# Performance work log

Measured on AMD Instinct MI355X. Metric: run time of the kernel, lower is better.

The kernel has to match this reference:

```python
import jax, jax.numpy as jnp
import numpy as np

MAX_REL = 2  # hard-coded max_relative_position in the torch module


def setup_inputs() -> dict:
    key = jax.random.key(0)
    ks = jax.random.split(key, 12)
    B, S, Dm, H = 2, 2048, 1024, 16
    D = Dm // H
    sc = 1.0 / np.sqrt(Dm)
    inp = {
        "x": jax.random.normal(ks[0], (B, S, Dm), jnp.float32),
        "Wq": jax.random.normal(ks[1], (Dm, Dm), jnp.float32) * sc,
        "bq": jnp.zeros((Dm,), jnp.float32),
        "Wk": jax.random.normal(ks[2], (Dm, Dm), jnp.float32) * sc,
        "bk": jnp.zeros((Dm,), jnp.float32),
        "Wv": jax.random.normal(ks[3], (Dm, Dm), jnp.float32) * sc,
        "bv": jnp.zeros((Dm,), jnp.float32),
        "Wo": jax.random.normal(ks[4], (Dm, Dm), jnp.float32) * sc,
        "bo": jnp.zeros((Dm,), jnp.float32),
        "rel_k": jax.random.normal(ks[5], (2 * MAX_REL + 1, D), jnp.float32) * 0.1,
        "rel_v": jax.random.normal(ks[6], (2 * MAX_REL + 1, D), jnp.float32) * 0.1,
        "num_heads": H,
    }
    return inp


def reference(x, Wq, bq, Wk, bk, Wv, bv, Wo, bo, rel_k, rel_v, num_heads):
    B, S, Dm = x.shape
    H = num_heads
    D = Dm // H
    n_buckets = 2 * MAX_REL + 1

    q = (x @ Wq + bq).reshape(B, S, H, D).transpose(0, 2, 1, 3)  # [B,H,S,D]
    k = (x @ Wk + bk).reshape(B, S, H, D).transpose(0, 2, 1, 3)
    v = (x @ Wv + bv).reshape(B, S, H, D).transpose(0, 2, 1, 3)

    # content-content scores
    attn1 = jnp.einsum('bhqd,bhkd->bhqk', q, k)

    # relative-position bucket index: clip(k - q, -MAX_REL, MAX_REL) + MAX_REL
    r = jnp.arange(S)
    idx = jnp.clip(r[None, :] - r[:, None], -MAX_REL, MAX_REL) + MAX_REL  # [S,S] int

    # content-position scores: q . rel_k[idx]  (project onto 5 buckets then gather)
    q_rel = jnp.einsum('bhqd,jd->bhqj', q, rel_k)  # [B,H,S,5]
    attn2 = jnp.take_along_axis(q_rel, jnp.broadcast_to(idx[None, None], (B, H, S, S)), axis=-1)

    scores = (attn1 + attn2) / jnp.sqrt(jnp.asarray(D, x.dtype))
    p = jax.nn.softmax(scores, axis=-1)  # dropout in eval mode -> identity

    out1 = jnp.einsum('bhqk,bhkd->bhqd', p, v)

    # position value term: sum_k p[...,k] * rel_v[idx[q,k]] via bucket accumulation
    onehot = (idx[:, :, None] == jnp.arange(n_buckets)[None, None, :]).astype(p.dtype)  # [S,S,5]
    bucket = jnp.einsum('bhqk,qkj->bhqj', p, onehot)
    out2 = jnp.einsum('bhqj,jd->bhqd', bucket, rel_v)

    out = (out1 + out2).transpose(0, 2, 1, 3).reshape(B, S, Dm)
    return out @ Wo + bo
```

## Files before the change

### kernel.cpp

```cpp
#include <hip/hip_runtime.h>

#define S_LEN 2048
#define DM    1024
#define NH    16
#define HD    64
#define BATCH 2
#define PPAD  2056

typedef __attribute__((ext_vector_type(8))) short short8;
typedef __attribute__((ext_vector_type(4))) float f32x4;

__device__ inline float b2f(unsigned short u) {
    return __uint_as_float(((unsigned)u) << 16);
}
__device__ inline unsigned short f2b(float f) {
    unsigned u = __float_as_uint(f);
    u += 0x7FFFu + ((u >> 16) & 1u);
    return (unsigned short)(u >> 16);
}
__device__ inline f32x4 zero4() {
    f32x4 z; z[0] = 0.f; z[1] = 0.f; z[2] = 0.f; z[3] = 0.f; return z;
}

__device__ inline size_t qk_frag_idx(int s, int d) {
    return (size_t)(s >> 4) * 1024 + (size_t)(d >> 5) * 512
         + (size_t)(((d & 31) >> 3) * 16 + (s & 15)) * 8 + (d & 7);
}
__device__ inline size_t v_frag_idx(int s, int d) {
    return (size_t)(s >> 5) * 2048 + (size_t)(d >> 4) * 512
         + (size_t)(((s & 31) >> 3) * 16 + (d & 15)) * 8 + (s & 7);
}
__device__ inline size_t af_idx(int m, int k) {
    return ((size_t)(m >> 4) * 32 + (size_t)(k >> 5)) * 512
         + (size_t)(((k & 31) >> 3) * 16 + (m & 15)) * 8 + (k & 7);
}

__global__ __launch_bounds__(256) void convert_w(
    const float* __restrict__ Wq, const float* __restrict__ Wk,
    const float* __restrict__ Wv, const float* __restrict__ Wo,
    unsigned short* __restrict__ Wf)
{
    int k = blockIdx.x, mat = blockIdx.y, tid = threadIdx.x;
    const float* W = (mat == 0) ? Wq : (mat == 1) ? Wk : (mat == 2) ? Wv : Wo;
    f32x4 w = *(const f32x4*)(W + (size_t)k * DM + tid * 4);
    unsigned short* dst = Wf + ((size_t)mat << 20);
#pragma unroll
    for (int e = 0; e < 4; e++) dst[af_idx(tid * 4 + e, k)] = f2b(w[e]);
}

__global__ __launch_bounds__(256) void convert_x(
    const float* __restrict__ x, unsigned short* __restrict__ Xf, int b)
{
    int m = blockIdx.x, tid = threadIdx.x;
    f32x4 v = *(const f32x4*)(x + ((size_t)b * S_LEN + m) * DM + tid * 4);
#pragma unroll
    for (int e = 0; e < 4; e++) Xf[af_idx(m, tid * 4 + e)] = f2b(v[e]);
}

__global__ __launch_bounds__(256) void proj_gemm_wf(
    const unsigned short* __restrict__ Xf,
    const unsigned short* __restrict__ Wf,
    const float* __restrict__ bq, const float* __restrict__ bk,
    const float* __restrict__ bv,
    unsigned short* __restrict__ Qs, unsigned short* __restrict__ Ks,
    unsigned short* __restrict__ Vts)
{
    int tid = threadIdx.x;
    int wave = tid >> 6, lane = tid & 63;
    int r = lane & 15, quad = lane >> 4;
    int mat = blockIdx.y >> 4;
    int hh  = blockIdx.y & 15;

    int mt0 = blockIdx.x * 8 + wave * 2;
    const unsigned short* A0 = Xf + (size_t)mt0 * 32 * 512 + lane * 8;
    const unsigned short* A1 = A0 + 32 * 512;
    const unsigned short* Bb = Wf + ((size_t)mat << 20)
                             + (size_t)(hh * 4) * 32 * 512 + lane * 8;

    f32x4 acc[2][4];
#pragma unroll
    for (int mt = 0; mt < 2; mt++)
#pragma unroll
        for (int nt = 0; nt < 4; nt++) acc[mt][nt] = zero4();

    short8 a0c = *(const short8*)A0;
    short8 a1c = *(const short8*)A1;
    short8 b0c = *(const short8*)(Bb);
    short8 b1c = *(const short8*)(Bb + 16384);
    short8 b2c = *(const short8*)(Bb + 32768);
    short8 b3c = *(const short8*)(Bb + 49152);

    for (int kt = 0; kt < 32; kt++) {
        short8 a0n, a1n, b0n, b1n, b2n, b3n;
        if (kt < 31) {
            size_t off = (size_t)(kt + 1) * 512;
            a0n = *(const short8*)(A0 + off);
            a1n = *(const short8*)(A1 + off);
            b0n = *(const short8*)(Bb + off);
            b1n = *(const short8*)(Bb + 16384 + off);
            b2n = *(const short8*)(Bb + 32768 + off);
            b3n = *(const short8*)(Bb + 49152 + off);
        }
        acc[0][0] = __builtin_amdgcn_mfma_f32_16x16x32_bf16(a0c, b0c, acc[0][0], 0, 0, 0);
        acc[0][1] = __builtin_amdgcn_mfma_f32_16x16x32_bf16(a0c, b1c, acc[0][1], 0, 0, 0);
        acc[0][2] = __builtin_amdgcn_mfma_f32_16x16x32_bf16(a0c, b2c, acc[0][2], 0, 0, 0);
        acc[0][3] = __builtin_amdgcn_mfma_f32_16x16x32_bf16(a0c, b3c, acc[0][3], 0, 0, 0);
        acc[1][0] = __builtin_amdgcn_mfma_f32_16x16x32_bf16(a1c, b0c, acc[1][0], 0, 0, 0);
        acc[1][1] = __builtin_amdgcn_mfma_f32_16x16x32_bf16(a1c, b1c, acc[1][1], 0, 0, 0);
        acc[1][2] = __builtin_amdgcn_mfma_f32_16x16x32_bf16(a1c, b2c, acc[1][2], 0, 0, 0);
        acc[1][3] = __builtin_amdgcn_mfma_f32_16x16x32_bf16(a1c, b3c, acc[1][3], 0, 0, 0);
        a0c = a0n; a1c = a1n;
        b0c = b0n; b1c = b1n; b2c = b2n; b3c = b3n;
    }

    const float* bias = (mat == 0) ? bq : (mat == 1) ? bk : bv;
    size_t hbase = (size_t)hh * S_LEN * HD;
    int gc0 = hh * 64;
#pragma unroll
    for (int mt = 0; mt < 2; mt++) {
#pragma unroll
        for (int nt = 0; nt < 4; nt++) {
            int d = nt * 16 + r;
            float bb = bias[gc0 + d];
#pragma unroll
            for (int i = 0; i < 4; i++) {
                int s = blockIdx.x * 128 + wave * 32 + mt * 16 + quad * 4 + i;
                float v = acc[mt][nt][i] + bb;
                if (mat == 2)      Vts[hbase + v_frag_idx(s, d)] = f2b(v);
                else if (mat == 0) Qs [hbase + qk_frag_idx(s, d)] = f2b(v);
                else               Ks [hbase + qk_frag_idx(s, d)] = f2b(v);
            }
        }
    }
}

__global__ __launch_bounds__(256) void outproj_wf(
    const unsigned short* __restrict__ AOf,
    const unsigned short* __restrict__ Wof,
    const float* __restrict__ bo,
    float* __restrict__ out, int b)
{
    int tid = threadIdx.x;
    int wave = tid >> 6, lane = tid & 63;
    int r = lane & 15, quad = lane >> 4;

    int mt0 = blockIdx.x * 8 + wave * 2;
    const unsigned short* A0 = AOf + (size_t)mt0 * 32 * 512 + lane * 8;
    const unsigned short* A1 = A0 + 32 * 512;
    const unsigned short* Bb = Wof + (size_t)(blockIdx.y * 4) * 32 * 512 + lane * 8;

    f32x4 acc[2][4];
#pragma unroll
    for (int mt = 0; mt < 2; mt++)
#pragma unroll
        for (int nt = 0; nt < 4; nt++) acc[mt][nt] = zero4();

    short8 a0c = *(const short8*)A0;
    short8 a1c = *(const short8*)A1;
    short8 b0c = *(const short8*)(Bb);
    short8 b1c = *(const short8*)(Bb + 16384);
    short8 b2c = *(const short8*)(Bb + 32768);
    short8 b3c = *(const short8*)(Bb + 49152);

    for (int kt = 0; kt < 32; kt++) {
        short8 a0n, a1n, b0n, b1n, b2n, b3n;
        if (kt < 31) {
            size_t off = (size_t)(kt + 1) * 512;
            a0n = *(const short8*)(A0 + off);
            a1n = *(const short8*)(A1 + off);
            b0n = *(const short8*)(Bb + off);
            b1n = *(const short8*)(Bb + 16384 + off);
            b2n = *(const short8*)(Bb + 32768 + off);
            b3n = *(const short8*)(Bb + 49152 + off);
        }
        acc[0][0] = __builtin_amdgcn_mfma_f32_16x16x32_bf16(a0c, b0c, acc[0][0], 0, 0, 0);
        acc[0][1] = __builtin_amdgcn_mfma_f32_16x16x32_bf16(a0c, b1c, acc[0][1], 0, 0, 0);
        acc[0][2] = __builtin_amdgcn_mfma_f32_16x16x32_bf16(a0c, b2c, acc[0][2], 0, 0, 0);
        acc[0][3] = __builtin_amdgcn_mfma_f32_16x16x32_bf16(a0c, b3c, acc[0][3], 0, 0, 0);
        acc[1][0] = __builtin_amdgcn_mfma_f32_16x16x32_bf16(a1c, b0c, acc[1][0], 0, 0, 0);
        acc[1][1] = __builtin_amdgcn_mfma_f32_16x16x32_bf16(a1c, b1c, acc[1][1], 0, 0, 0);
        acc[1][2] = __builtin_amdgcn_mfma_f32_16x16x32_bf16(a1c, b2c, acc[1][2], 0, 0, 0);
        acc[1][3] = __builtin_amdgcn_mfma_f32_16x16x32_bf16(a1c, b3c, acc[1][3], 0, 0, 0);
        a0c = a0n; a1c = a1n;
        b0c = b0n; b1c = b1n; b2c = b2n; b3c = b3n;
    }

#pragma unroll
    for (int mt = 0; mt < 2; mt++) {
#pragma unroll
        for (int nt = 0; nt < 4; nt++) {
            int n = blockIdx.y * 64 + nt * 16 + r;
            float bb = bo[n];
#pragma unroll
            for (int i = 0; i < 4; i++) {
                int m = blockIdx.x * 128 + wave * 32 + mt * 16 + quad * 4 + i;
                out[((size_t)b * S_LEN + m) * DM + n] = acc[mt][nt][i] + bb;
            }
        }
    }
}

__global__ __launch_bounds__(256) void proj_fused_xf(
    const unsigned short* __restrict__ Xf,
    const float* __restrict__ Wq, const float* __restrict__ Wk,
    const float* __restrict__ Wv,
    const float* __restrict__ bq, const float* __restrict__ bk,
    const float* __restrict__ bv,
    unsigned short* __restrict__ Qs, unsigned short* __restrict__ Ks,
    unsigned short* __restrict__ Vts)
{
    __shared__ unsigned short Bs[64][72];

    int tid = threadIdx.x;
    int wave = tid >> 6, lane = tid & 63;
    int r = lane & 15, quad = lane >> 4;
    int m0 = blockIdx.x * 64 + wave * 16;
    int mat = blockIdx.y / NH;
    int hh  = blockIdx.y % NH;
    int gc0 = hh * 64;

    const float* W    = (mat == 0) ? Wq : (mat == 1) ? Wk : Wv;
    const float* bias = (mat == 0) ? bq : (mat == 1) ? bk : bv;

    f32x4 acc[4];
#pragma unroll
    for (int nt = 0; nt < 4; nt++) acc[nt] = zero4();

    int kr = tid >> 2;
    int nc = (tid & 3) * 16;
    const unsigned short* Af = Xf + (size_t)(blockIdx.x * 4 + wave) * 32 * 512 + lane * 8;

    for (int k0 = 0; k0 < DM; k0 += 64) {
        const f32x4* wr = (const f32x4*)(W + (size_t)(k0 + kr) * DM + gc0 + nc);
        f32x4 w0 = wr[0], w1 = wr[1], w2 = wr[2], w3 = wr[3];
        __syncthreads();
        Bs[nc +  0][kr] = f2b(w0[0]); Bs[nc +  1][kr] = f2b(w0[1]);
        Bs[nc +  2][kr] = f2b(w0[2]); Bs[nc +  3][kr] = f2b(w0[3]);
        Bs[nc +  4][kr] = f2b(w1[0]); Bs[nc +  5][kr] = f2b(w1[1]);
        Bs[nc +  6][kr] = f2b(w1[2]); Bs[nc +  7][kr] = f2b(w1[3]);
        Bs[nc +  8][kr] = f2b(w2[0]); Bs[nc +  9][kr] = f2b(w2[1]);
        Bs[nc + 10][kr] = f2b(w2[2]); Bs[nc + 11][kr] = f2b(w2[3]);
        Bs[nc + 12][kr] = f2b(w3[0]); Bs[nc + 13][kr] = f2b(w3[1]);
        Bs[nc + 14][kr] = f2b(w3[2]); Bs[nc + 15][kr] = f2b(w3[3]);
        __syncthreads();

#pragma unroll
        for (int ks = 0; ks < 2; ks++) {
            int kt = (k0 >> 5) + ks;
            short8 a = *(const short8*)(Af + (size_t)kt * 512);
#pragma unroll
            for (int nt = 0; nt < 4; nt++) {
                short8 bf = *(const short8*)&Bs[nt * 16 + r][ks * 32 + quad * 8];
                acc[nt] = __builtin_amdgcn_mfma_f32_16x16x32_bf16(a, bf, acc[nt], 0, 0, 0);
            }
        }
    }

    size_t hbase = (size_t)hh * S_LEN * HD;
#pragma unroll
    for (int nt = 0; nt < 4; nt++) {
        int d = nt * 16 + r;
        float bb = bias[gc0 + d];
#pragma unroll
        for (int i = 0; i < 4; i++) {
            int s = m0 + quad * 4 + i;
            float v = acc[nt][i] + bb;
            if (mat == 2)      Vts[hbase + v_frag_idx(s, d)] = f2b(v);
            else if (mat == 0) Qs [hbase + qk_frag_idx(s, d)] = f2b(v);
            else               Ks [hbase + qk_frag_idx(s, d)] = f2b(v);
        }
    }
}

__global__ __launch_bounds__(256) void proj_fused_legacy(
    const float* __restrict__ x,
    const float* __restrict__ Wq, const float* __restrict__ Wk,
    const float* __restrict__ Wv,
    const float* __restrict__ bq, const float* __restrict__ bk,
    const float* __restrict__ bv,
    unsigned short* __restrict__ Qs, unsigned short* __restrict__ Ks,
    unsigned short* __restrict__ Vts,
    int b, int head0, int NG)
{
    __shared__ unsigned short Bs[64][72];

    int tid = threadIdx.x;
    int wave = tid >> 6, lane = tid & 63;
    int r = lane & 15, quad = lane >> 4;
    int m0 = blockIdx.x * 64 + wave * 16;
    int mat = blockIdx.y / NG;
    int hh  = blockIdx.y % NG;
    int gc0 = (head0 + hh) * 64;

    const float* W    = (mat == 0) ? Wq : (mat == 1) ? Wk : Wv;
    const float* bias = (mat == 0) ? bq : (mat == 1) ? bk : bv;
    const float* xb = x + (size_t)b * S_LEN * DM;

    f32x4 acc[4];
#pragma unroll
    for (int nt = 0; nt < 4; nt++) acc[nt] = zero4();

    int kr = tid >> 2;
    int nc = (tid & 3) * 16;
    const float* am = xb + (size_t)(m0 + r) * DM + quad * 8;

    for (int k0 = 0; k0 < DM; k0 += 64) {
        const f32x4* wr = (const f32x4*)(W + (size_t)(k0 + kr) * DM + gc0 + nc);
        f32x4 w0 = wr[0], w1 = wr[1], w2 = wr[2], w3 = wr[3];
        __syncthreads();
        Bs[nc +  0][kr] = f2b(w0[0]); Bs[nc +  1][kr] = f2b(w0[1]);
        Bs[nc +  2][kr] = f2b(w0[2]); Bs[nc +  3][kr] = f2b(w0[3]);
        Bs[nc +  4][kr] = f2b(w1[0]); Bs[nc +  5][kr] = f2b(w1[1]);
        Bs[nc +  6][kr] = f2b(w1[2]); Bs[nc +  7][kr] = f2b(w1[3]);
        Bs[nc +  8][kr] = f2b(w2[0]); Bs[nc +  9][kr] = f2b(w2[1]);
        Bs[nc + 10][kr] = f2b(w2[2]); Bs[nc + 11][kr] = f2b(w2[3]);
        Bs[nc + 12][kr] = f2b(w3[0]); Bs[nc + 13][kr] = f2b(w3[1]);
        Bs[nc + 14][kr] = f2b(w3[2]); Bs[nc + 15][kr] = f2b(w3[3]);
        __syncthreads();

#pragma unroll
        for (int ks = 0; ks < 2; ks++) {
            const f32x4* ap = (const f32x4*)(am + k0 + ks * 32);
            f32x4 a0 = ap[0], a1 = ap[1];
            short8 a;
            a[0] = (short)f2b(a0[0]); a[1] = (short)f2b(a0[1]);
            a[2] = (short)f2b(a0[2]); a[3] = (short)f2b(a0[3]);
            a[4] = (short)f2b(a1[0]); a[5] = (short)f2b(a1[1]);
            a[6] = (short)f2b(a1[2]); a[7] = (short)f2b(a1[3]);
#pragma unroll
            for (int nt = 0; nt < 4; nt++) {
                short8 bf = *(const short8*)&Bs[nt * 16 + r][ks * 32 + quad * 8];
                acc[nt] = __builtin_amdgcn_mfma_f32_16x16x32_bf16(a, bf, acc[nt], 0, 0, 0);
            }
        }
    }

    size_t hbase = (size_t)hh * S_LEN * HD;
#pragma unroll
    for (int nt = 0; nt < 4; nt++) {
        int d = nt * 16 + r;
        float bb = bias[gc0 + d];
#pragma unroll
        for (int i = 0; i < 4; i++) {
            int s = m0 + quad * 4 + i;
            float v = acc[nt][i] + bb;
            if (mat == 2)      Vts[hbase + v_frag_idx(s, d)] = f2b(v);
            else if (mat == 0) Qs [hbase + qk_frag_idx(s, d)] = f2b(v);
            else               Ks [hbase + qk_frag_idx(s, d)] = f2b(v);
        }
    }
}

__global__ __launch_bounds__(1024, 8) void attn_mfma(
    const unsigned short* __restrict__ Q,
    const unsigned short* __restrict__ Km,
    const unsigned short* __restrict__ Vt,
    const float* __restrict__ relk,
    const float* __restrict__ relv,
    unsigned short* __restrict__ Aout,
    int col_base,
    int NG, int ao_frag)
{
    __shared__ alignas(16) unsigned short pmat[16][PPAD];
    __shared__ float qrel_s[16][5];
    __shared__ float relv_s[5][HD];
    __shared__ float rowstat[16][8];
    __shared__ float wden[16][16];
    __shared__ float wsuf[16][16];

    int tid = threadIdx.x;
    int wave = tid >> 6, lane = tid & 63;
    int r = lane & 15, quad = lane >> 4;

    int bid = blockIdx.x;
    int hh, jq;
    if (NG == 16) {
        int xcd = bid & 7, j = bid >> 3;
        hh = xcd + ((j >> 7) << 3);
        jq = j & 127;
    } else {
        hh = bid >> 7;
        jq = bid & 127;
    }
    int q0 = jq << 4;

    size_t qk_base = (size_t)hh * S_LEN * HD;
    size_t v_base  = (size_t)hh * S_LEN * HD;

    const unsigned short* qf = Q + qk_base + (size_t)(q0 >> 4) * 1024 + lane * 8;
    short8 aq0 = *(const short8*)qf;
    short8 aq1 = *(const short8*)(qf + 512);

    {
        int t2 = tid - 64;
        if (t2 >= 0 && t2 < 5 * HD) relv_s[t2 >> 6][t2 & 63] = relv[t2];
    }

    if (wave == 0) {
#pragma unroll
        for (int j = 0; j < 5; j++) {
            const f32x4* rk0 = (const f32x4*)(relk + j * HD + quad * 8);
            const f32x4* rk1 = (const f32x4*)(relk + j * HD + 32 + quad * 8);
            f32x4 r0a = rk0[0], r0b = rk0[1], r1a = rk1[0], r1b = rk1[1];
            float s = 0.f;
#pragma unroll
            for (int e = 0; e < 4; e++) {
                s += b2f((unsigned short)aq0[e])     * r0a[e];
                s += b2f((unsigned short)aq0[e + 4]) * r0b[e];
                s += b2f((unsigned short)aq1[e])     * r1a[e];
                s += b2f((unsigned short)aq1[e + 4]) * r1b[e];
            }
            s += __shfl_xor(s, 16);
            s += __shfl_xor(s, 32);
            if (quad == 0) qrel_s[r][j] = s;
        }
    }

    __syncthreads();

    float dpart[4] = {0.f, 0.f, 0.f, 0.f};
    float spart[4] = {0.f, 0.f, 0.f, 0.f};
    int rowq = quad * 4;

    const unsigned short* kb = Km + qk_base + (size_t)(wave * 8) * 1024 + lane * 8;
    short8 bk0 = *(const short8*)kb;
    short8 bk1 = *(const short8*)(kb + 512);

    for (int t = 0; t < 8; t++) {
        short8 nb0, nb1;
        if (t < 7) {
            const unsigned short* kn = kb + (size_t)(t + 1) * 1024;
            nb0 = *(const short8*)(kn);
            nb1 = *(const short8*)(kn + 512);
        }
        f32x4 a1 = zero4();
        a1 = __builtin_amdgcn_mfma_f32_16x16x32_bf16(aq0, bk0, a1, 0, 0, 0);
        a1 = __builtin_amdgcn_mfma_f32_16x16x32_bf16(aq1, bk1, a1, 0, 0, 0);
        int col = wave * 128 + t * 16 + r;
#pragma unroll
        for (int i = 0; i < 4; i++) {
            int row = rowq + i;
            int qglob = q0 + row;
            int del = min(2, max(-2, col - qglob));
            float s = (a1[i] + qrel_s[row][del + 2]) * 0.125f;
            float e = __expf(s);
            pmat[row][col] = f2b(e);
            dpart[i] += e;
            if (col >= qglob + 2) spart[i] += e;
        }
        bk0 = nb0; bk1 = nb1;
    }
#pragma unroll
    for (int off = 1; off <= 8; off <<= 1) {
#pragma unroll
        for (int i = 0; i < 4; i++) {
            dpart[i] += __shfl_xor(dpart[i], off);
            spart[i] += __shfl_xor(spart[i], off);
        }
    }
    if (r == 0) {
#pragma unroll
        for (int i = 0; i < 4; i++) {
            wden[wave][rowq + i] = dpart[i];
            wsuf[wave][rowq + i] = spart[i];
        }
    }
    __syncthreads();

    if (tid < 16) {
        int row = tid, qglob = q0 + row;
        float denom = 0.f, suf = 0.f;
        for (int w = 0; w < 16; w++) { denom += wden[w][row]; suf += wsuf[w][row]; }
        float b1  = (qglob >= 1) ? b2f(pmat[row][qglob - 1]) : 0.f;
        float b2v = b2f(pmat[row][qglob]);
        float b3  = (qglob + 1 < S_LEN) ? b2f(pmat[row][qglob + 1]) : 0.f;
        rowstat[row][0] = 1.f / denom;
        rowstat[row][1] = denom - suf - b1 - b2v - b3;
        rowstat[row][2] = b1;
        rowstat[row][3] = b2v;
        rowstat[row][4] = b3;
        rowstat[row][5] = suf;
    }
    __syncthreads();

    {
        int nt = wave & 3, kc = wave >> 2;
        f32x4 oacc = zero4();
        const unsigned short* vf = Vt + v_base + (size_t)(kc * 16) * 2048
                                 + (size_t)nt * 512 + lane * 8;
        short8 af = *(const short8*)&pmat[r][kc * 512 + quad * 8];
        short8 bv = *(const short8*)vf;
        for (int st = 0; st < 16; st++) {
            short8 afn, bvn;
            if (st < 15) {
                afn = *(const short8*)&pmat[r][kc * 512 + (st + 1) * 32 + quad * 8];
                bvn = *(const short8*)(vf + (size_t)(st + 1) * 2048);
            }
            oacc = __builtin_amdgcn_mfma_f32_16x16x32_bf16(af, bv, oacc, 0, 0, 0);
            af = afn; bv = bvn;
        }
        __syncthreads();
        float* pbuf = (float*)&pmat[0][0];
#pragma unroll
        for (int i = 0; i < 4; i++)
            pbuf[((size_t)kc * 16 + quad * 4 + i) * 65 + nt * 16 + r] = oacc[i];
    }
    __syncthreads();

    {
        const float* pbuf = (const float*)&pmat[0][0];
        int orow = tid >> 6, ocol = tid & 63;
        float o = pbuf[(0 * 16 + orow) * 65 + ocol] + pbuf[(1 * 16 + orow) * 65 + ocol]
                + pbuf[(2 * 16 + orow) * 65 + ocol] + pbuf[(3 * 16 + orow) * 65 + ocol];
        float o2 = rowstat[orow][1] * relv_s[0][ocol]
                 + rowstat[orow][2] * relv_s[1][ocol]
                 + rowstat[orow][3] * relv_s[2][ocol]
                 + rowstat[orow][4] * relv_s[3][ocol]
                 + rowstat[orow][5] * relv_s[4][ocol];
        float res = (o + o2) * rowstat[orow][0];
        int col = col_base + hh * HD + ocol;
        if (ao_frag)
            Aout[af_idx(q0 + orow, col)] = f2b(res);
        else
            Aout[(size_t)(q0 + orow) * DM + col] = f2b(res);
    }
}

__global__ __launch_bounds__(256) void outproj_fused(
    const unsigned short* __restrict__ AO,
    const float* __restrict__ Wo,
    const float* __restrict__ bo,
    float* __restrict__ out, int b)
{
    __shared__ unsigned short Bs[64][72];

    int tid = threadIdx.x;
    int wave = tid >> 6, lane = tid & 63;
    int r = lane & 15, quad = lane >> 4;
    int m0 = blockIdx.x * 64 + wave * 16;
    int n0 = blockIdx.y * 64;

    f32x4 acc[4];
#pragma unroll
    for (int nt = 0; nt < 4; nt++) acc[nt] = zero4();

    int kr = tid >> 2;
    int nc = (tid & 3) * 16;
    const short8* ap = (const short8*)(AO + (size_t)(m0 + r) * DM + quad * 8);

    for (int k0 = 0; k0 < DM; k0 += 64) {
        const f32x4* wr = (const f32x4*)(Wo + (size_t)(k0 + kr) * DM + n0 + nc);
        f32x4 w0 = wr[0], w1 = wr[1], w2 = wr[2], w3 = wr[3];
        __syncthreads();
        Bs[nc +  0][kr] = f2b(w0[0]); Bs[nc +  1][kr] = f2b(w0[1]);
        Bs[nc +  2][kr] = f2b(w0[2]); Bs[nc +  3][kr] = f2b(w0[3]);
        Bs[nc +  4][kr] = f2b(w1[0]); Bs[nc +  5][kr] = f2b(w1[1]);
        Bs[nc +  6][kr] = f2b(w1[2]); Bs[nc +  7][kr] = f2b(w1[3]);
        Bs[nc +  8][kr] = f2b(w2[0]); Bs[nc +  9][kr] = f2b(w2[1]);
        Bs[nc + 10][kr] = f2b(w2[2]); Bs[nc + 11][kr] = f2b(w2[3]);
        Bs[nc + 12][kr] = f2b(w3[0]); Bs[nc + 13][kr] = f2b(w3[1]);
        Bs[nc + 14][kr] = f2b(w3[2]); Bs[nc + 15][kr] = f2b(w3[3]);
        __syncthreads();

#pragma unroll
        for (int ks = 0; ks < 2; ks++) {
            short8 a = ap[ks * 4];
#pragma unroll
            for (int nt = 0; nt < 4; nt++) {
                short8 bf = *(const short8*)&Bs[nt * 16 + r][ks * 32 + quad * 8];
                acc[nt] = __builtin_amdgcn_mfma_f32_16x16x32_bf16(a, bf, acc[nt], 0, 0, 0);
            }
        }
        ap += 8;
    }

#pragma unroll
    for (int nt = 0; nt < 4; nt++) {
        int n = n0 + nt * 16 + r;
        float bb = bo[n];
#pragma unroll
        for (int i = 0; i < 4; i++) {
            int m = m0 + quad * 4 + i;
            out[((size_t)b * S_LEN + m) * DM + n] = acc[nt][i] + bb;
        }
    }
}

extern "C" void kernel_launch(void* const* d_in, const int* in_sizes, int n_in,
                              void* d_out, int out_size, void* d_ws, size_t ws_size,
                              hipStream_t stream)
{
    const float* x  = (const float*)d_in[0];
    const float* Wq = (const float*)d_in[1];
    const float* bq = (const float*)d_in[2];
    const float* Wk = (const float*)d_in[3];
    const float* bk = (const float*)d_in[4];
    const float* Wv = (const float*)d_in[5];
    const float* bv = (const float*)d_in[6];
    const float* Wo = (const float*)d_in[7];
    const float* bo = (const float*)d_in[8];
    const float* rk = (const float*)d_in[9];
    const float* rv = (const float*)d_in[10];
    float* outp = (float*)d_out;

    unsigned short* ws = (unsigned short*)d_ws;
    const size_t M1 = 1048576;

    if (ws_size >= (size_t)25165824) {
        unsigned short* Wf   = ws;
        unsigned short* XfAO = ws + 4 * M1;
        unsigned short* Qs   = ws + 6 * M1;
        unsigned short* Ks   = ws + 8 * M1;
        unsigned short* Vts  = ws + 10 * M1;

        convert_w<<<dim3(1024, 4), 256, 0, stream>>>(Wq, Wk, Wv, Wo, Wf);
        for (int b = 0; b < BATCH; b++) {
            convert_x<<<dim3(2048), 256, 0, stream>>>(x, XfAO, b);
            proj_gemm_wf<<<dim3(16, 48), 256, 0, stream>>>(
                XfAO, Wf, bq, bk, bv, Qs, Ks, Vts);
            attn_mfma<<<dim3(2048), 1024, 0, stream>>>(
                Qs, Ks, Vts, rk, rv, XfAO, 0, 16, 1);
            outproj_wf<<<dim3(16, 16), 256, 0, stream>>>(
                XfAO, Wf + 3 * M1, bo, outp, b);
        }
    } else if (ws_size >= (size_t)16777216) {
        unsigned short* XfAO = ws;
        unsigned short* Qs   = ws + 2 * M1;
        unsigned short* Ks   = ws + 4 * M1;
        unsigned short* Vts  = ws + 6 * M1;

        for (int b = 0; b < BATCH; b++) {
            convert_x<<<dim3(2048), 256, 0, stream>>>(x, XfAO, b);
            proj_fused_xf<<<dim3(32, 48), 256, 0, stream>>>(
                XfAO, Wq, Wk, Wv, bq, bk, bv, Qs, Ks, Vts);
            attn_mfma<<<dim3(2048), 1024, 0, stream>>>(
                Qs, Ks, Vts, rk, rv, XfAO, 0, 16, 0);
            outproj_fused<<<dim3(32, 16), 256, 0, stream>>>(XfAO, Wo, bo, outp, b);
        }
    } else {
        const int NG = 4;
        const size_t slice = (size_t)NG * S_LEN * HD;
        unsigned short* Qs  = ws;
        unsigned short* Ks  = ws + slice;
        unsigned short* Vts = ws + 2 * slice;
        unsigned short* AOb = ws + 3 * slice;

        for (int b = 0; b < BATCH; b++) {
            for (int g = 0; g < NH / NG; g++) {
                int head0 = g * NG;
                proj_fused_legacy<<<dim3(32, 3 * NG), 256, 0, stream>>>(
                    x, Wq, Wk, Wv, bq, bk, bv, Qs, Ks, Vts, b, head0, NG);
                attn_mfma<<<dim3((S_LEN / 16) * NG), 1024, 0, stream>>>(
                    Qs, Ks, Vts, rk, rv, AOb, head0 * HD, NG, 0);
            }
            outproj_fused<<<dim3(32, 16), 256, 0, stream>>>(AOb, Wo, bo, outp, b);
        }
    }
}
```

Baseline: 327.3 us.

## Keep P in registers and fuse PV MFMA into QK loop per wave

The attention kernel no longer writes the full bf16 probability matrix to shared memory. Each wave computes S^T tiles with swapped MFMA operands, converts the exponentials to packed bf16, shuffles them into A-operand layout and immediately accumulates P·V over its own key slice. The per-wave partial outputs are then reduced through a float shared buffer, and the diagonal bucket values are captured directly. Off-diagonal tiles use a fast path with a precomputed exp2 scale and a constant rel-k bias. This removes the large LDS write/read round trip and a barrier phase, at the cost of extra cross-lane shuffles, a 16-way reduction and a larger output buffer.

```diff
diff --git a/kernel.cpp b/kernel.cpp
--- a/kernel.cpp
+++ b/kernel.cpp
@@ -5,7 +5,6 @@
 #define NH    16
 #define HD    64
 #define BATCH 2
-#define PPAD  2056
 
 typedef __attribute__((ext_vector_type(8))) short short8;
 typedef __attribute__((ext_vector_type(4))) float f32x4;
@@ -351,6 +350,40 @@
     }
 }
 
+#define QK_TILE(T, EE)                                                        \
+    {                                                                         \
+        short8 bk0 = *(const short8*)(kb + (size_t)(T) * 1024);               \
+        short8 bk1 = *(const short8*)(kb + (size_t)(T) * 1024 + 512);         \
+        f32x4 sACC = zero4();                                                 \
+        sACC = __builtin_amdgcn_mfma_f32_16x16x32_bf16(bk0, aq0, sACC, 0, 0, 0); \
+        sACC = __builtin_amdgcn_mfma_f32_16x16x32_bf16(bk1, aq1, sACC, 0, 0, 0); \
+        int c0 = wave * 128 + (T) * 16;                                       \
+        if (c0 + 17 <= q0) {                                                  \
+            _Pragma("unroll")                                                 \
+            for (int i = 0; i < 4; i++) {                                     \
+                float e = __builtin_amdgcn_exp2f(__fmaf_rn(sACC[i], C, qlo)); \
+                EE[i] = e; dpart += e;                                        \
+            }                                                                 \
+        } else if (c0 >= q0 + 17) {                                           \
+            _Pragma("unroll")                                                 \
+            for (int i = 0; i < 4; i++) {                                     \
+                float e = __builtin_amdgcn_exp2f(__fmaf_rn(sACC[i], C, qhi)); \
+                EE[i] = e; dpart += e; spart += e;                            \
+            }                                                                 \
+        } else {                                                              \
+            _Pragma("unroll")                                                 \
+            for (int i = 0; i < 4; i++) {                                     \
+                int col = c0 + quad * 4 + i;                                  \
+                int del = min(2, max(-2, col - qglob));                       \
+                float e = __builtin_amdgcn_exp2f((sACC[i] + qrel_s[r][del + 2]) * C); \
+                EE[i] = e; dpart += e;                                        \
+                if (col >= qglob + 2) spart += e;                             \
+                int dd = col - qglob;                                         \
+                if (dd >= -1 && dd <= 1) diag_s[r][dd + 1] = e;               \
+            }                                                                 \
+        }                                                                     \
+    }
+
 __global__ __launch_bounds__(1024, 8) void attn_mfma(
     const unsigned short* __restrict__ Q,
     const unsigned short* __restrict__ Km,
@@ -361,12 +394,13 @@
     int col_base,
     int NG, int ao_frag)
 {
-    __shared__ alignas(16) unsigned short pmat[16][PPAD];
+    __shared__ float obuf[16][16][66];
     __shared__ float qrel_s[16][5];
     __shared__ float relv_s[5][HD];
     __shared__ float rowstat[16][8];
     __shared__ float wden[16][16];
     __shared__ float wsuf[16][16];
+    __shared__ float diag_s[16][4];
 
     int tid = threadIdx.x;
     int wave = tid >> 6, lane = tid & 63;
@@ -385,12 +419,12 @@
     int q0 = jq << 4;
 
     size_t qk_base = (size_t)hh * S_LEN * HD;
-    size_t v_base  = (size_t)hh * S_LEN * HD;
 
     const unsigned short* qf = Q + qk_base + (size_t)(q0 >> 4) * 1024 + lane * 8;
     short8 aq0 = *(const short8*)qf;
     short8 aq1 = *(const short8*)(qf + 512);
 
+    if (tid >= 384 && tid < 448) diag_s[(tid - 384) >> 2][(tid - 384) & 3] = 0.f;
     {
         int t2 = tid - 64;
         if (t2 >= 0 && t2 < 5 * HD) relv_s[t2 >> 6][t2 & 63] = relv[t2];
@@ -418,62 +452,70 @@
 
     __syncthreads();
 
-    float dpart[4] = {0.f, 0.f, 0.f, 0.f};
-    float spart[4] = {0.f, 0.f, 0.f, 0.f};
-    int rowq = quad * 4;
+    const float C = 0.18033688f;
+    float dpart = 0.f, spart = 0.f;
+    float qlo = qrel_s[r][0] * C;
+    float qhi = qrel_s[r][4] * C;
+    int qglob = q0 + r;
+
+    f32x4 oacc[4];
+#pragma unroll
+    for (int nt = 0; nt < 4; nt++) oacc[nt] = zero4();
 
     const unsigned short* kb = Km + qk_base + (size_t)(wave * 8) * 1024 + lane * 8;
-    short8 bk0 = *(const short8*)kb;
-    short8 bk1 = *(const short8*)(kb + 512);
-
-    for (int t = 0; t < 8; t++) {
-        short8 nb0, nb1;
-        if (t < 7) {
-            const unsigned short* kn = kb + (size_t)(t + 1) * 1024;
-            nb0 = *(const short8*)(kn);
-            nb1 = *(const short8*)(kn + 512);
-        }
-        f32x4 a1 = zero4();
-        a1 = __builtin_amdgcn_mfma_f32_16x16x32_bf16(aq0, bk0, a1, 0, 0, 0);
-        a1 = __builtin_amdgcn_mfma_f32_16x16x32_bf16(aq1, bk1, a1, 0, 0, 0);
-        int col = wave * 128 + t * 16 + r;
-#pragma unroll
-        for (int i = 0; i < 4; i++) {
-            int row = rowq + i;
-            int qglob = q0 + row;
-            int del = min(2, max(-2, col - qglob));
-            float s = (a1[i] + qrel_s[row][del + 2]) * 0.125f;
-            float e = __expf(s);
-            pmat[row][col] = f2b(e);
-            dpart[i] += e;
-            if (col >= qglob + 2) spart[i] += e;
-        }
-        bk0 = nb0; bk1 = nb1;
-    }
-#pragma unroll
-    for (int off = 1; off <= 8; off <<= 1) {
-#pragma unroll
-        for (int i = 0; i < 4; i++) {
-            dpart[i] += __shfl_xor(dpart[i], off);
-            spart[i] += __shfl_xor(spart[i], off);
-        }
-    }
-    if (r == 0) {
-#pragma unroll
-        for (int i = 0; i < 4; i++) {
-            wden[wave][rowq + i] = dpart[i];
-            wsuf[wave][rowq + i] = spart[i];
-        }
-    }
+    const unsigned short* vb = Vt + qk_base + (size_t)(wave * 4) * 2048 + lane * 8;
+
+#pragma unroll 1
+    for (int u = 0; u < 4; u++) {
+        float e0[4], e1[4];
+        QK_TILE(u * 2,     e0);
+        QK_TILE(u * 2 + 1, e1);
+
+        unsigned Au, Bu, Cu, Du;
+        asm("v_cvt_pk_bf16_f32 %0, %1, %2" : "=v"(Au) : "v"(e0[0]), "v"(e0[1]));
+        asm("v_cvt_pk_bf16_f32 %0, %1, %2" : "=v"(Bu) : "v"(e0[2]), "v"(e0[3]));
+        asm("v_cvt_pk_bf16_f32 %0, %1, %2" : "=v"(Cu) : "v"(e1[0]), "v"(e1[1]));
+        asm("v_cvt_pk_bf16_f32 %0, %1, %2" : "=v"(Du) : "v"(e1[2]), "v"(e1[3]));
+        unsigned A2 = __shfl_xor(Au, 32), B2 = __shfl_xor(Bu, 32);
+        unsigned C2 = __shfl_xor(Cu, 32), D2 = __shfl_xor(Du, 32);
+        bool low = (lane < 32);
+        unsigned M  = low ? Au : C2, N  = low ? Bu : D2;
+        unsigned P  = low ? A2 : Cu, Qw = low ? B2 : Du;
+        unsigned M2 = __shfl_xor(M, 16), N2 = __shfl_xor(N, 16);
+        unsigned P2 = __shfl_xor(P, 16), Q2 = __shfl_xor(Qw, 16);
+        bool even = ((lane & 16) == 0);
+        union { unsigned u32[4]; short8 s8; } pa;
+        pa.u32[0] = even ? M  : P2;
+        pa.u32[1] = even ? N  : Q2;
+        pa.u32[2] = even ? M2 : P;
+        pa.u32[3] = even ? N2 : Qw;
+
+        const unsigned short* vc = vb + (size_t)u * 2048;
+#pragma unroll
+        for (int nt = 0; nt < 4; nt++) {
+            short8 bv = *(const short8*)(vc + (size_t)nt * 512);
+            oacc[nt] = __builtin_amdgcn_mfma_f32_16x16x32_bf16(pa.s8, bv, oacc[nt], 0, 0, 0);
+        }
+    }
+
+    dpart += __shfl_xor(dpart, 16); dpart += __shfl_xor(dpart, 32);
+    spart += __shfl_xor(spart, 16); spart += __shfl_xor(spart, 32);
+    if (lane < 16) { wden[wave][r] = dpart; wsuf[wave][r] = spart; }
+
+#pragma unroll
+    for (int nt = 0; nt < 4; nt++)
+#pragma unroll
+        for (int i = 0; i < 4; i++)
+            obuf[wave][quad * 4 + i][nt * 16 + r] = oacc[nt][i];
     __syncthreads();
 
     if (tid < 16) {
-        int row = tid, qglob = q0 + row;
+        int row = tid;
         float denom = 0.f, suf = 0.f;
         for (int w = 0; w < 16; w++) { denom += wden[w][row]; suf += wsuf[w][row]; }
-        float b1  = (qglob >= 1) ? b2f(pmat[row][qglob - 1]) : 0.f;
-        float b2v = b2f(pmat[row][qglob]);
-        float b3  = (qglob + 1 < S_LEN) ? b2f(pmat[row][qglob + 1]) : 0.f;
+        float b1  = diag_s[row][0];
+        float b2v = diag_s[row][1];
+        float b3  = diag_s[row][2];
         rowstat[row][0] = 1.f / denom;
         rowstat[row][1] = denom - suf - b1 - b2v - b3;
         rowstat[row][2] = b1;
@@ -484,34 +526,10 @@
     __syncthreads();
 
     {
-        int nt = wave & 3, kc = wave >> 2;
-        f32x4 oacc = zero4();
-        const unsigned short* vf = Vt + v_base + (size_t)(kc * 16) * 2048
-                                 + (size_t)nt * 512 + lane * 8;
-        short8 af = *(const short8*)&pmat[r][kc * 512 + quad * 8];
-        short8 bv = *(const short8*)vf;
-        for (int st = 0; st < 16; st++) {
-            short8 afn, bvn;
-            if (st < 15) {
-                afn = *(const short8*)&pmat[r][kc * 512 + (st + 1) * 32 + quad * 8];
-                bvn = *(const short8*)(vf + (size_t)(st + 1) * 2048);
-            }
-            oacc = __builtin_amdgcn_mfma_f32_16x16x32_bf16(af, bv, oacc, 0, 0, 0);
-            af = afn; bv = bvn;
-        }
-        __syncthreads();
-        float* pbuf = (float*)&pmat[0][0];
-#pragma unroll
-        for (int i = 0; i < 4; i++)
-            pbuf[((size_t)kc * 16 + quad * 4 + i) * 65 + nt * 16 + r] = oacc[i];
-    }
-    __syncthreads();
-
-    {
-        const float* pbuf = (const float*)&pmat[0][0];
         int orow = tid >> 6, ocol = tid & 63;
-        float o = pbuf[(0 * 16 + orow) * 65 + ocol] + pbuf[(1 * 16 + orow) * 65 + ocol]
-                + pbuf[(2 * 16 + orow) * 65 + ocol] + pbuf[(3 * 16 + orow) * 65 + ocol];
+        float o = 0.f;
+#pragma unroll
+        for (int w = 0; w < 16; w++) o += obuf[w][orow][ocol];
         float o2 = rowstat[orow][1] * relv_s[0][ocol]
                  + rowstat[orow][2] * relv_s[1][ocol]
                  + rowstat[orow][3] * relv_s[2][ocol]
```

Measured after the change: 312.8 us. 1.05x faster.
